# Kernel tuning notes

Hardware: AMD Instinct MI355X
Metric: run time of the kernel (lower is better)

Reference implementation:

```python
import jax, jax.numpy as jnp
import numpy as np

N = 50000        # nodes
E = 800000       # directed edges
NUM_E = 10000    # hyperedges
NFEAT, NHID, NOUT = 256, 128, 64
K = 10
TEMP = 5.0


def gcn_prop(h, src, dst, n):
    # PyG GCNConv propagation with added self-loops: D^-1/2 (A+I) D^-1/2 h
    ew = jnp.ones(src.shape[0], h.dtype)
    deg = 1.0 + jax.ops.segment_sum(ew, dst, num_segments=n)  # self-loop adds 1
    dinv = jax.lax.rsqrt(deg)
    norm = dinv[src] * dinv[dst]                   # [E]
    out = jax.ops.segment_sum(h[src] * norm[:, None], dst, num_segments=n)
    out = out + h / deg[:, None]                   # self-loop term (weight deg^-1)
    return out


def gcn_conv(x, W, b, src, dst, n):
    return gcn_prop(x @ W, src, dst, n) + b


def hgnnp_conv(x, W, b, hv, he, n, num_e):
    # dhg HGNNPConv: theta(x) then v->e mean aggregation, then e->v mean
    h = x @ W + b
    ones = jnp.ones(hv.shape[0], h.dtype)
    e_deg = jnp.maximum(jax.ops.segment_sum(ones, he, num_segments=num_e), 1.0)
    v_deg = jnp.maximum(jax.ops.segment_sum(ones, hv, num_segments=n), 1.0)
    e_feat = jax.ops.segment_sum(h[hv], he, num_segments=num_e) / e_deg[:, None]
    v_out = jax.ops.segment_sum(e_feat[he], hv, num_segments=n) / v_deg[:, None]
    return v_out


def setup_inputs() -> dict:
    key = jax.random.key(0)
    ks = jax.random.split(key, 12)
    x = jax.random.normal(ks[0], (N, NFEAT), jnp.float32)
    edge_index = jax.random.randint(ks[1], (2, E), 0, N)
    hv_idx = jax.random.randint(ks[2], (200000,), 0, N)
    he_idx = jax.random.randint(ks[3], (200000,), 0, NUM_E)

    def glorot(k, shape):
        lim = float(np.sqrt(6.0 / (shape[0] + shape[1])))
        return jax.random.uniform(k, shape, jnp.float32, -lim, lim)

    return {
        "x": x, "edge_index": edge_index, "hv_idx": hv_idx, "he_idx": he_idx,
        "gcn_W1": glorot(ks[4], (NFEAT, NHID)), "gcn_b1": jnp.zeros((NHID,), jnp.float32),
        "gcn_W2": glorot(ks[5], (NHID, NOUT)), "gcn_b2": jnp.zeros((NOUT,), jnp.float32),
        "hg_W1": glorot(ks[6], (NFEAT, NHID)), "hg_b1": jnp.zeros((NHID,), jnp.float32),
        "hg_W2": glorot(ks[7], (NHID, NOUT)), "hg_b2": jnp.zeros((NOUT,), jnp.float32),
        "num_iter": 1,
    }


def reference(x, edge_index, hv_idx, he_idx,
              gcn_W1, gcn_b1, gcn_W2, gcn_b2,
              hg_W1, hg_b1, hg_W2, hg_b2, num_iter):
    src, dst = edge_index[0], edge_index[1]

    # HGNNP_GCN encoder (dropout is identity in eval-style reference)
    x1 = jax.nn.relu(gcn_conv(x, gcn_W1, gcn_b1, src, dst, N))
    x2 = gcn_conv(x1, gcn_W2, gcn_b2, src, dst, N)
    x3 = jax.nn.relu(hgnnp_conv(x, hg_W1, hg_b1, hv_idx, he_idx, N, NUM_E))
    x4 = hgnnp_conv(x3, hg_W2, hg_b2, hv_idx, he_idx, N, NUM_E)  # is_last: no act
    embeds = x2 * 0.5 + x4 * 0.5                     # [N, NOUT]

    # row-normalize (diag(1/||row||) @ data)
    data = embeds / jnp.linalg.norm(embeds, axis=1, keepdims=True)

    # kmeans++ init is a host-side, data-dependent pick; use deterministic
    # strided row selection from the (detached) normalized embeddings.
    init_idx = jnp.arange(K) * (N // K)
    mu = jax.lax.stop_gradient(data[init_idx])       # [K, NOUT]

    for _ in range(int(num_iter)):
        dist = data @ mu.T                           # [N, K]
        r = jax.nn.softmax(TEMP * dist, axis=1)
        cluster_r = r.sum(axis=0)                    # [K]
        cluster_mean = r.T @ data                    # [K, NOUT]
        mu = cluster_mean / cluster_r[:, None]

    dist = data @ mu.T
    r = jax.nn.softmax(TEMP * dist, axis=1)
    return mu, r, embeds, dist
```

## Files before the change

### kernel.cpp

```cpp
#include <hip/hip_runtime.h>
#include <hip/hip_bf16.h>


#define NN   50000
#define NP   50048
#define EE   800000
#define NINC 200000
#define NEH  10000
#define KCL  10
#define CBLK 782

#define MU_OFF  0
#define R_OFF   640
#define EMB_OFF 500640
#define D_OFF   3700640

typedef __hip_bfloat16 bf16;
typedef unsigned short u16;
typedef unsigned int   u32;
typedef __attribute__((ext_vector_type(8))) short short8;
typedef __attribute__((ext_vector_type(4))) float f32x4;

__device__ __forceinline__ float b2f(bf16 v){ return __bfloat162float(v); }
__device__ __forceinline__ float us2f(u16 u){ return __uint_as_float(((unsigned)u) << 16); }
__device__ __forceinline__ u16 f2bu(float f){
  unsigned u = __float_as_uint(f);
  return (u16)((u + 0x7fffu + ((u >> 16) & 1u)) >> 16);
}
__device__ __forceinline__ bf16 f2b(float f){
  u16 r = f2bu(f);
  bf16 h;
  reinterpret_cast<u16&>(h) = r;
  return h;
}
__device__ __forceinline__ float ldf(const void* p, size_t i, int isbf){
  return isbf ? b2f(((const bf16*)p)[i]) : ((const float*)p)[i];
}
__device__ __forceinline__ void stf(void* p, size_t i, float v, int isbf){
  if (isbf) ((bf16*)p)[i] = f2b(v);
  else      ((float*)p)[i] = v;
}

__global__ void k_detect(const u16* __restrict__ xr, int* flag){
  __shared__ int bad;
  if (threadIdx.x == 0) bad = 0;
  __syncthreads();
  for (int i = threadIdx.x; i < 4096; i += 256){
    int e = (xr[i] >> 7) & 0xFF;
    if (e >= 0xEF) bad = 1;
  }
  __syncthreads();
  if (threadIdx.x == 0) *flag = bad ? 0 : 1;
}

__global__ void k_aconv(const void* __restrict__ x, u16* __restrict__ xb,
                        const int* __restrict__ flag){
  int i = blockIdx.x*256 + threadIdx.x;
  const int n4 = NN*256/4;
  if (i >= n4) return;
  ushort4 o;
  if (flag[0]){
    o = ((const ushort4*)x)[i];
  } else {
    float4 v = ((const float4*)x)[i];
    o = make_ushort4(f2bu(v.x), f2bu(v.y), f2bu(v.z), f2bu(v.w));
  }
  ((ushort4*)xb)[i] = o;
}

__global__ void k_wprep(const void* gW1, const void* hW1, const void* gW2, const void* hW2,
                        const void* gb1, const void* hb1, const void* gb2, const void* hb2,
                        u16* gW1t, u16* hW1t, u16* gW2t, u16* hW2t,
                        float* gb1f, float* hb1f, float* gb2f, float* hb2f,
                        const int* __restrict__ flag){
  const int isbf = flag[0];
  int i = blockIdx.x*256 + threadIdx.x;
  if (i < 256*128){
    int n = i >> 8, k = i & 255;
    gW1t[i] = f2bu(ldf(gW1, (size_t)k*128 + n, isbf));
    hW1t[i] = f2bu(ldf(hW1, (size_t)k*128 + n, isbf));
  }
  if (i < 64*128){
    int n = i >> 7, k = i & 127;
    gW2t[i] = f2bu(ldf(gW2, (size_t)k*64 + n, isbf));
    hW2t[i] = f2bu(ldf(hW2, (size_t)k*64 + n, isbf));
  }
  if (i < 128){ gb1f[i] = ldf(gb1,i,isbf); hb1f[i] = ldf(hb1,i,isbf); }
  if (i < 64) { gb2f[i] = ldf(gb2,i,isbf); hb2f[i] = ldf(hb2,i,isbf); }
}

template<int NBKT, int NPB>
__global__ __launch_bounds__(256) void k_histA(const int* __restrict__ key,
                                               int* __restrict__ HA, int chunk){
  __shared__ u32 hist[NBKT];
  for (int i = threadIdx.x; i < NBKT; i += 256) hist[i] = 0;
  __syncthreads();
  int base = blockIdx.x*chunk;
  for (int i = threadIdx.x; i < chunk; i += 256)
    atomicAdd(&hist[key[base+i]/NPB], 1u);
  __syncthreads();
  int* out = HA + blockIdx.x*NBKT;
  for (int i = threadIdx.x; i < NBKT; i += 256) out[i] = (int)hist[i];
}

__global__ void k_scanA_all(int* HAg, int* HAv, int* HAe,
                            int* bsg, int* bsv, int* bse){
  int* HA; int* bs; int nch;
  if (blockIdx.x == 0){ HA = HAg; bs = bsg; nch = 128; }
  else if (blockIdx.x == 1){ HA = HAv; bs = bsv; nch = 64; }
  else { HA = HAe; bs = bse; nch = 64; }
  __shared__ int s[256];
  int t = threadIdx.x;
  int run = 0;
  if (t < 250){
    for (int c = 0; c < nch; ++c){
      int v = HA[c*250 + t];
      HA[c*250 + t] = run;
      run += v;
    }
  }
  int own = (t < 250) ? run : 0;
  s[t] = own; __syncthreads();
  #pragma unroll
  for (int off = 1; off < 256; off <<= 1){
    int add = (t >= off) ? s[t-off] : 0;
    __syncthreads();
    s[t] += add;
    __syncthreads();
  }
  if (t < 250) bs[t] = s[t] - own;
  if (t == 255) bs[250] = s[255];
}

template<int NBKT, int NPB>
__global__ __launch_bounds__(256) void k_fillA(const int* __restrict__ key,
    const int* __restrict__ val, const int* __restrict__ HA,
    const int* __restrict__ bs, u32* __restrict__ packed, int chunk){
  __shared__ u32 cur[NBKT];
  const int* pre = HA + blockIdx.x*NBKT;
  for (int i = threadIdx.x; i < NBKT; i += 256) cur[i] = (u32)(bs[i] + pre[i]);
  __syncthreads();
  int base = blockIdx.x*chunk;
  for (int i = threadIdx.x; i < chunk; i += 256){
    int k = key[base+i];
    int b = k / NPB;
    u32 pos = atomicAdd(&cur[b], 1u);
    packed[pos] = ((u32)(k - b*NPB) << 16) | (u32)val[base+i];
  }
}

template<int NPB>
__global__ __launch_bounds__(256) void k_fillB(const u32* __restrict__ packed,
    const int* __restrict__ bs, int* __restrict__ csr,
    int* __restrict__ cnt, int* __restrict__ rp){
  __shared__ u32 hist[NPB];
  __shared__ int s[256];
  __shared__ u32 cur[NPB];
  const int b = blockIdx.x;
  const int s0 = bs[b], m = bs[b+1] - s0;
  const int t = threadIdx.x;
  for (int i = t; i < NPB; i += 256) hist[i] = 0;
  __syncthreads();
  for (int i = t; i < m; i += 256)
    atomicAdd(&hist[packed[s0+i] >> 16], 1u);
  __syncthreads();
  int own = (t < NPB) ? (int)hist[t] : 0;
  s[t] = own; __syncthreads();
  #pragma unroll
  for (int off = 1; off < 256; off <<= 1){
    int add = (t >= off) ? s[t-off] : 0;
    __syncthreads();
    s[t] += add;
    __syncthreads();
  }
  if (t < NPB){
    int excl = s[t] - own;
    cnt[b*NPB + t] = own;
    rp[b*NPB + t]  = s0 + excl;
    cur[t] = (u32)(s0 + excl);
  }
  __syncthreads();
  for (int i = t; i < m; i += 256){
    u32 p = packed[s0+i];
    u32 pos = atomicAdd(&cur[p >> 16], 1u);
    csr[pos] = (int)(p & 0xffffu);
  }
}

__global__ void k_invs(const int* __restrict__ cg, const int* __restrict__ cv,
                       const int* __restrict__ ce,
                       float* dinv, float* invv, float* inve){
  int i = blockIdx.x*256 + threadIdx.x;
  if (i < NN){
    float d = 1.0f + (float)cg[i];
    dinv[i] = rsqrtf(d);
    invv[i] = 1.0f / fmaxf((float)cv[i], 1.0f);
  } else if (i < NP){
    dinv[i] = 0.f;
  }
  if (i < NEH) inve[i] = 1.0f / fmaxf((float)ce[i], 1.0f);
}

template<int KDIM, int NCOL>
__global__ __launch_bounds__(256) void k_gemm_mfma(
    const u16* __restrict__ A, const u16* __restrict__ Wt,
    const float* __restrict__ bias, const float* __restrict__ rowscale,
    u16* __restrict__ C, int relu)
{
  constexpr int NT  = NCOL/16;
  constexpr int LDA = 40;
  __shared__ __align__(16) u16 Asl[64][LDA];
  __shared__ __align__(16) u16 Wsl[NCOL][LDA];
  const int tid  = threadIdx.x;
  const int wave = tid >> 6, lane = tid & 63;
  const int l15 = lane & 15, l4 = lane >> 4;
  const int row0 = blockIdx.x * 64;
  const int ar = tid >> 2, aq = tid & 3;
  constexpr int NW = NCOL*4/256;

  f32x4 acc[NT] = {};

  for (int kk = 0; kk < KDIM; kk += 32){
    {
      uint4 v = *(const uint4*)(A + (size_t)(row0 + ar)*KDIM + kk + aq*8);
      *(uint4*)&Asl[ar][aq*8] = v;
    }
    #pragma unroll
    for (int w2 = 0; w2 < NW; ++w2){
      int c = tid + w2*256;
      int n = c >> 2, q = c & 3;
      uint4 v = *(const uint4*)(Wt + (size_t)n*KDIM + kk + q*8);
      *(uint4*)&Wsl[n][q*8] = v;
    }
    __syncthreads();
    short8 af = *(const short8*)&Asl[wave*16 + l15][l4*8];
    #pragma unroll
    for (int t = 0; t < NT; ++t){
      short8 bf = *(const short8*)&Wsl[t*16 + l15][l4*8];
      acc[t] = __builtin_amdgcn_mfma_f32_16x16x32_bf16(af, bf, acc[t], 0, 0, 0);
    }
    __syncthreads();
  }

  #pragma unroll
  for (int t = 0; t < NT; ++t){
    int gcol = t*16 + l15;
    float b = bias ? bias[gcol] : 0.f;
    #pragma unroll
    for (int e = 0; e < 4; ++e){
      int grow = row0 + wave*16 + l4*4 + e;
      float v = acc[t][e] + b;
      if (relu) v = fmaxf(v, 0.f);
      if (rowscale) v *= rowscale[grow];
      C[(size_t)grow*NCOL + gcol] = f2bu(v);
    }
  }
}

template<int F, bool OUTBF, bool SELF>
__global__ __launch_bounds__(256) void k_gather(
    const int* __restrict__ rp, const int* __restrict__ cnt,
    const int* __restrict__ csr, const float* __restrict__ scale,
    const u16* __restrict__ h, const float* __restrict__ bias,
    void* __restrict__ out, int relu)
{
  const int wave = threadIdx.x >> 6, lane = threadIdx.x & 63;
  const int d = blockIdx.x*4 + wave;
  const int k0 = rp[d], n = cnt[d];

  if constexpr (F == 128){
    const uint* h32 = (const uint*)h;
    float a0=0,a1=0,b0=0,b1=0,c0=0,c1=0,e0=0,e1=0;
    if (SELF){
      uint v = h32[(size_t)d*64 + lane];
      a0 = us2f((u16)v); a1 = us2f((u16)(v>>16));
    }
    for (int base = 0; base < n; base += 64){
      int mm = n - base; if (mm > 64) mm = 64;
      int idx = (lane < mm) ? csr[k0 + base + lane] : 0;
      int jj = 0;
      for (; jj + 4 <= mm; jj += 4){
        int s0=__shfl(idx,jj), s1=__shfl(idx,jj+1), s2=__shfl(idx,jj+2), s3=__shfl(idx,jj+3);
        uint v0 = h32[(size_t)s0*64 + lane];
        uint v1 = h32[(size_t)s1*64 + lane];
        uint v2 = h32[(size_t)s2*64 + lane];
        uint v3 = h32[(size_t)s3*64 + lane];
        a0 += us2f((u16)v0); a1 += us2f((u16)(v0>>16));
        b0 += us2f((u16)v1); b1 += us2f((u16)(v1>>16));
        c0 += us2f((u16)v2); c1 += us2f((u16)(v2>>16));
        e0 += us2f((u16)v3); e1 += us2f((u16)(v3>>16));
      }
      for (; jj < mm; ++jj){
        int s = __shfl(idx, jj);
        uint v = h32[(size_t)s*64 + lane];
        a0 += us2f((u16)v); a1 += us2f((u16)(v>>16));
      }
    }
    float sc = scale[d];
    float o0 = ((a0+b0)+(c0+e0))*sc;
    float o1 = ((a1+b1)+(c1+e1))*sc;
    if (bias){ o0 += bias[lane*2]; o1 += bias[lane*2+1]; }
    if (relu){ o0 = fmaxf(o0,0.f); o1 = fmaxf(o1,0.f); }
    if (OUTBF){
      ((uint*)out)[(size_t)d*64 + lane] = (uint)f2bu(o0) | ((uint)f2bu(o1) << 16);
    } else {
      ((float2*)out)[(size_t)d*64 + lane] = make_float2(o0, o1);
    }
  } else {
    float a=0,b=0,c=0,e=0;
    if (SELF) a = us2f(h[(size_t)d*64 + lane]);
    for (int base = 0; base < n; base += 64){
      int mm = n - base; if (mm > 64) mm = 64;
      int idx = (lane < mm) ? csr[k0 + base + lane] : 0;
      int jj = 0;
      for (; jj + 4 <= mm; jj += 4){
        int s0=__shfl(idx,jj), s1=__shfl(idx,jj+1), s2=__shfl(idx,jj+2), s3=__shfl(idx,jj+3);
        a += us2f(h[(size_t)s0*64 + lane]);
        b += us2f(h[(size_t)s1*64 + lane]);
        c += us2f(h[(size_t)s2*64 + lane]);
        e += us2f(h[(size_t)s3*64 + lane]);
      }
      for (; jj < mm; ++jj){
        int s = __shfl(idx, jj);
        a += us2f(h[(size_t)s*64 + lane]);
      }
    }
    float o = ((a+b)+(c+e))*scale[d];
    if (bias) o += bias[lane];
    if (relu) o = fmaxf(o, 0.f);
    if (OUTBF) ((u16*)out)[(size_t)d*64 + lane] = f2bu(o);
    else       ((float*)out)[(size_t)d*64 + lane] = o;
  }
}

__global__ void k_embeds(const float* __restrict__ x2, const float* __restrict__ x4,
                         void* __restrict__ out, float* __restrict__ data,
                         const int* __restrict__ flag){
  int row  = blockIdx.x*4 + (threadIdx.x >> 6);
  int lane = threadIdx.x & 63;
  if (row >= NN) return;
  size_t idx = (size_t)row*64 + lane;
  float v = 0.5f*(x2[idx] + x4[idx]);
  float ss = v*v;
  #pragma unroll
  for (int off=32; off>0; off>>=1) ss += __shfl_xor(ss, off);
  float inv = rsqrtf(ss);
  data[idx] = v*inv;
  stf(out, EMB_OFF + idx, v, flag[0]);
}

__global__ void k_mu_init(const float* __restrict__ data, float* __restrict__ mu){
  int p = blockIdx.x*256 + threadIdx.x;
  if (p >= KCL*64) return;
  int k = p >> 6, f = p & 63;
  mu[p] = data[(size_t)k*(NN/KCL)*64 + f];
}

__global__ __launch_bounds__(640) void k_cluster_iter(const float* __restrict__ data,
    const float* __restrict__ mu, float* __restrict__ part, float* __restrict__ pcr,
    const int* __restrict__ nit, int iter)
{
  if (iter >= nit[0]) return;
  __shared__ float ms[640];
  __shared__ float dt[64][65];
  __shared__ float ds[64][11];
  const int tid = threadIdx.x;
  ms[tid] = mu[tid];
  const int base = blockIdx.x*64;
  for (int i = tid; i < 4096; i += 640){
    int r = i >> 6, f = i & 63;
    int grow = base + r;
    dt[r][f] = (grow < NN) ? data[(size_t)grow*64 + f] : 0.f;
  }
  __syncthreads();
  {
    const int row = tid & 63, k = tid >> 6;
    float dot = 0.f;
    #pragma unroll 16
    for (int f = 0; f < 64; ++f)
      dot = fmaf(dt[row][f], ms[k*64 + f], dot);
    ds[row][k] = dot;
  }
  __syncthreads();
  if (tid < 64){
    float dot[KCL];
    #pragma unroll
    for (int k = 0; k < KCL; ++k) dot[k] = ds[tid][k];
    float m = -1e30f;
    #pragma unroll
    for (int k = 0; k < KCL; ++k) m = fmaxf(m, 5.0f*dot[k]);
    float s = 0.f, ev[KCL];
    #pragma unroll
    for (int k = 0; k < KCL; ++k){ ev[k] = expf(5.0f*dot[k]-m); s += ev[k]; }
    float inv = (base + tid < NN) ? 1.0f/s : 0.f;
    #pragma unroll
    for (int k = 0; k < KCL; ++k) ds[tid][k] = ev[k]*inv;
  }
  __syncthreads();
  {
    const int f = tid & 63, k = tid >> 6;
    float acc = 0.f, crp = 0.f;
    #pragma unroll 8
    for (int t = 0; t < 64; ++t){
      float rv = ds[t][k];
      acc = fmaf(rv, dt[t][f], acc);
      crp += rv;
    }
    part[(size_t)blockIdx.x*640 + tid] = acc;
    if (f == 0) pcr[blockIdx.x*16 + k] = crp;
  }
}

__global__ void k_cred1(const float* __restrict__ part, const float* __restrict__ pcr,
                        float* __restrict__ p2, float* __restrict__ pc2,
                        const int* __restrict__ nit, int iter){
  if (iter >= nit[0]) return;
  int b = blockIdx.x, t = threadIdx.x;
  int r0 = b*20, r1 = r0 + 20; if (r1 > CBLK) r1 = CBLK;
  if (t < 640){
    float a = 0.f;
    for (int r = r0; r < r1; ++r) a += part[(size_t)r*640 + t];
    p2[(size_t)b*640 + t] = a;
  } else if (t < 640 + KCL){
    int k = t - 640;
    float a = 0.f;
    for (int r = r0; r < r1; ++r) a += pcr[r*16 + k];
    pc2[b*16 + k] = a;
  }
}

__global__ void k_cred2(const float* __restrict__ p2, const float* __restrict__ pc2,
                        float* __restrict__ csum, float* __restrict__ cr,
                        const int* __restrict__ nit, int iter){
  if (iter >= nit[0]) return;
  int t = threadIdx.x;
  if (t < 640){
    float a = 0.f;
    #pragma unroll
    for (int b = 0; b < 40; ++b) a += p2[(size_t)b*640 + t];
    csum[t] = a;
  } else if (t < 640 + KCL){
    int k = t - 640;
    float a = 0.f;
    #pragma unroll
    for (int b = 0; b < 40; ++b) a += pc2[b*16 + k];
    cr[k] = a;
  }
}

__global__ void k_mu_update(float* __restrict__ mu, const float* __restrict__ csum,
                            const float* __restrict__ cr,
                            const int* __restrict__ nit, int iter){
  if (iter >= nit[0]) return;
  int p = threadIdx.x;
  mu[p] = csum[p] / cr[p >> 6];
}

__global__ __launch_bounds__(640) void k_cluster_final(const float* __restrict__ data,
    const float* __restrict__ mu, void* __restrict__ out, const int* __restrict__ flag)
{
  __shared__ float ms[640];
  __shared__ float dt[64][65];
  __shared__ float ds[64][11];
  const int tid = threadIdx.x;
  ms[tid] = mu[tid];
  const int base = blockIdx.x*64;
  for (int i = tid; i < 4096; i += 640){
    int r = i >> 6, f = i & 63;
    int grow = base + r;
    dt[r][f] = (grow < NN) ? data[(size_t)grow*64 + f] : 0.f;
  }
  __syncthreads();
  {
    const int row = tid & 63, k = tid >> 6;
    float dot = 0.f;
    #pragma unroll 16
    for (int f = 0; f < 64; ++f)
      dot = fmaf(dt[row][f], ms[k*64 + f], dot);
    ds[row][k] = dot;
  }
  __syncthreads();
  if (tid < 64 && base + tid < NN){
    const int row = base + tid;
    const int isbf = flag[0];
    float dot[KCL];
    #pragma unroll
    for (int k = 0; k < KCL; ++k) dot[k] = ds[tid][k];
    float m = -1e30f;
    #pragma unroll
    for (int k = 0; k < KCL; ++k) m = fmaxf(m, 5.0f*dot[k]);
    float s = 0.f, ev[KCL];
    #pragma unroll
    for (int k = 0; k < KCL; ++k){ ev[k] = expf(5.0f*dot[k]-m); s += ev[k]; }
    float inv = 1.0f/s;
    #pragma unroll
    for (int k = 0; k < KCL; ++k){
      stf(out, (size_t)D_OFF + (size_t)row*KCL + k, dot[k],    isbf);
      stf(out, (size_t)R_OFF + (size_t)row*KCL + k, ev[k]*inv, isbf);
    }
  }
}

__global__ void k_mu_out(const float* __restrict__ mu, void* __restrict__ out,
                         const int* __restrict__ flag){
  int p = blockIdx.x*256 + threadIdx.x;
  if (p < KCL*64) stf(out, MU_OFF + p, mu[p], flag[0]);
}

extern "C" void kernel_launch(void* const* d_in, const int* in_sizes, int n_in,
                              void* d_out, int out_size, void* d_ws, size_t ws_size,
                              hipStream_t stream)
{
  const void* x   = d_in[0];
  const int*  ei  = (const int*)d_in[1];
  const int*  hv  = (const int*)d_in[2];
  const int*  he  = (const int*)d_in[3];
  const void* gW1 = d_in[4];
  const void* gb1 = d_in[5];
  const void* gW2 = d_in[6];
  const void* gb2 = d_in[7];
  const void* hW1 = d_in[8];
  const void* hb1 = d_in[9];
  const void* hW2 = d_in[10];
  const void* hb2 = d_in[11];
  const int*  nit = (const int*)d_in[12];

  float* ws = (float*)d_ws;
  size_t o = 0;
  u16*   xb  = (u16*)(ws + o); o += (size_t)NP*128;
  u16*   BAb = (u16*)(ws + o); o += (size_t)NP*64;
  u16*   BBb = (u16*)(ws + o); o += (size_t)NP*64;
  u16*   BCb = (u16*)(ws + o); o += (size_t)NP*64;
  u16*   BDb = (u16*)(ws + o); o += (size_t)NEH*64;
  u16*  gW1t = (u16*)(ws + o); o += 16384;
  u16*  hW1t = (u16*)(ws + o); o += 16384;
  u16*  gW2t = (u16*)(ws + o); o += 4096;
  u16*  hW2t = (u16*)(ws + o); o += 4096;
  float* gb1f = ws + o; o += 128;
  float* hb1f = ws + o; o += 128;
  float* gb2f = ws + o; o += 64;
  float* hb2f = ws + o; o += 64;
  float* dinv = ws + o; o += 50048;
  float* invv = ws + o; o += 50048;
  float* inve = ws + o; o += 10048;
  float* mu   = ws + o; o += 640;
  float* csum = ws + o; o += 640;
  float* cr   = ws + o; o += 64;
  float* part = ws + o; o += (size_t)CBLK*640;
  float* pcr  = ws + o; o += CBLK*16;
  float* p2   = ws + o; o += 40*640;
  float* pc2  = ws + o; o += 40*16;
  int*   dflg = (int*)(ws + o); o += 16;
  float* x2f   = (float*)xb;
  float* x4f   = (float*)xb + (size_t)NP*64;
  float* dataf = (float*)BBb;
  int* ib = (int*)(ws + o);
  size_t io = 0;
  int* cg    = ib + io; io += NN;
  int* cv    = ib + io; io += NN;
  int* ce    = ib + io; io += NEH + 48;
  int* rp_g  = ib + io; io += NN;
  int* rp_v  = ib + io; io += NN;
  int* rp_e  = ib + io; io += NEH + 48;
  int* csr_g = ib + io; io += EE;
  int* csr_e = ib + io; io += NINC;
  int* csr_v = ib + io; io += NINC;
  int* HAg   = ib + io; io += 128*250;
  int* HAv   = ib + io; io += 64*250;
  int* HAe   = ib + io; io += 64*250;
  int* bsg   = ib + io; io += 256;
  int* bsv   = ib + io; io += 256;
  int* bse   = ib + io; io += 256;
  u32* pg = (u32*)(ib + io); io += EE;
  u32* pv = (u32*)(ib + io); io += NINC;
  u32* pe = (u32*)(ib + io); io += NINC;

  const int* srcp = ei;
  const int* dstp = ei + EE;
  dim3 B(256);
  const int NBP = (NP + 255)/256;

  k_detect<<<dim3(1), B, 0, stream>>>((const u16*)x, dflg);
  k_aconv<<<dim3(12500), B, 0, stream>>>(x, xb, dflg);
  k_wprep<<<dim3(128), B, 0, stream>>>(gW1, hW1, gW2, hW2, gb1, hb1, gb2, hb2,
                                       gW1t, hW1t, gW2t, hW2t,
                                       gb1f, hb1f, gb2f, hb2f, dflg);

  k_histA<250,200><<<dim3(128), B, 0, stream>>>(dstp, HAg, 6250);
  k_histA<250,200><<<dim3(64),  B, 0, stream>>>(hv,   HAv, 3125);
  k_histA<250, 40><<<dim3(64),  B, 0, stream>>>(he,   HAe, 3125);
  k_scanA_all<<<dim3(3), B, 0, stream>>>(HAg, HAv, HAe, bsg, bsv, bse);
  k_fillA<250,200><<<dim3(128), B, 0, stream>>>(dstp, srcp, HAg, bsg, pg, 6250);
  k_fillA<250,200><<<dim3(64),  B, 0, stream>>>(hv,   he,   HAv, bsv, pv, 3125);
  k_fillA<250, 40><<<dim3(64),  B, 0, stream>>>(he,   hv,   HAe, bse, pe, 3125);
  k_fillB<200><<<dim3(250), B, 0, stream>>>(pg, bsg, csr_g, cg, rp_g);
  k_fillB<200><<<dim3(250), B, 0, stream>>>(pv, bsv, csr_v, cv, rp_v);
  k_fillB< 40><<<dim3(250), B, 0, stream>>>(pe, bse, csr_e, ce, rp_e);
  k_invs<<<dim3(NBP), B, 0, stream>>>(cg, cv, ce, dinv, invv, inve);

  const int NB = NP/64;
  k_gemm_mfma<256,128><<<dim3(NB), B, 0, stream>>>(xb, gW1t, nullptr, dinv, BAb, 0);
  k_gather<128,true,true><<<dim3(NN/4), B, 0, stream>>>(rp_g, cg, csr_g, dinv,
                                                        BAb, gb1f, BBb, 1);
  k_gemm_mfma<256,128><<<dim3(NB), B, 0, stream>>>(xb, hW1t, hb1f, nullptr, BAb, 0);
  k_gather<128,true,false><<<dim3(NEH/4), B, 0, stream>>>(rp_e, ce, csr_e, inve,
                                                          BAb, nullptr, BDb, 0);
  k_gather<128,true,false><<<dim3(NN/4), B, 0, stream>>>(rp_v, cv, csr_v, invv,
                                                         BDb, nullptr, BCb, 1);
  k_gemm_mfma<128,64><<<dim3(NB), B, 0, stream>>>(BBb, gW2t, nullptr, dinv, BAb, 0);
  k_gather<64,false,true><<<dim3(NN/4), B, 0, stream>>>(rp_g, cg, csr_g, dinv,
                                                        BAb, gb2f, x2f, 0);
  k_gemm_mfma<128,64><<<dim3(NB), B, 0, stream>>>(BCb, hW2t, hb2f, nullptr, BAb, 0);
  k_gather<64,true,false><<<dim3(NEH/4), B, 0, stream>>>(rp_e, ce, csr_e, inve,
                                                         BAb, nullptr, BDb, 0);
  k_gather<64,false,false><<<dim3(NN/4), B, 0, stream>>>(rp_v, cv, csr_v, invv,
                                                         BDb, nullptr, x4f, 0);

  k_embeds<<<dim3((NN+3)/4), B, 0, stream>>>(x2f, x4f, d_out, dataf, dflg);

  k_mu_init<<<dim3(3), B, 0, stream>>>(dataf, mu);
  for (int it = 0; it < 4; ++it){
    k_cluster_iter<<<dim3(CBLK), dim3(640), 0, stream>>>(dataf, mu, part, pcr, nit, it);
    k_cred1       <<<dim3(40),   dim3(768), 0, stream>>>(part, pcr, p2, pc2, nit, it);
    k_cred2       <<<dim3(1),    dim3(768), 0, stream>>>(p2, pc2, csum, cr, nit, it);
    k_mu_update   <<<dim3(1),    dim3(640), 0, stream>>>(mu, csum, cr, nit, it);
  }
  k_cluster_final<<<dim3(CBLK), dim3(640), 0, stream>>>(dataf, mu, d_out, dflg);
  k_mu_out       <<<dim3(3),  B, 0, stream>>>(mu, d_out, dflg);
}
```

Baseline: 372.3 us.

## Merge independent GCN and hypergraph stages into shared launches to cut kernel count

Merges independent kernels into combined launches that dispatch on block index. Input and weight prep become one launch, and the three histogram, fillA and fillB passes each become one launch, with the degree-inverse computation folded into fillB. The GCN and hypergraph GEMM and gather stages are paired so that independent branches run in the same grid, using an extra buffer BEb to break the write conflicts. The cluster reduce and mu update are fused, and the mu output write moves into the final kernel. This removes about 20 launches and their serialization gaps, at the cost of mixed-workload grids where GEMM and gather blocks share one register and LDS budget.

```diff
diff --git a/kernel.cpp b/kernel.cpp
--- a/kernel.cpp
+++ b/kernel.cpp
@@ -53,54 +53,58 @@
   if (threadIdx.x == 0) *flag = bad ? 0 : 1;
 }
 
-__global__ void k_aconv(const void* __restrict__ x, u16* __restrict__ xb,
-                        const int* __restrict__ flag){
-  int i = blockIdx.x*256 + threadIdx.x;
-  const int n4 = NN*256/4;
-  if (i >= n4) return;
-  ushort4 o;
-  if (flag[0]){
-    o = ((const ushort4*)x)[i];
+__global__ __launch_bounds__(256) void k_prep(const void* __restrict__ x, u16* __restrict__ xb,
+    const void* gW1, const void* hW1, const void* gW2, const void* hW2,
+    const void* gb1, const void* hb1, const void* gb2, const void* hb2,
+    u16* gW1t, u16* hW1t, u16* gW2t, u16* hW2t,
+    float* gb1f, float* hb1f, float* gb2f, float* hb2f,
+    const int* __restrict__ flag){
+  const int isbf = flag[0];
+  const int blk = blockIdx.x;
+  if (blk < 12500){
+    int i = blk*256 + threadIdx.x;
+    ushort4 o;
+    if (isbf){
+      o = ((const ushort4*)x)[i];
+    } else {
+      float4 v = ((const float4*)x)[i];
+      o = make_ushort4(f2bu(v.x), f2bu(v.y), f2bu(v.z), f2bu(v.w));
+    }
+    ((ushort4*)xb)[i] = o;
   } else {
-    float4 v = ((const float4*)x)[i];
-    o = make_ushort4(f2bu(v.x), f2bu(v.y), f2bu(v.z), f2bu(v.w));
-  }
-  ((ushort4*)xb)[i] = o;
-}
-
-__global__ void k_wprep(const void* gW1, const void* hW1, const void* gW2, const void* hW2,
-                        const void* gb1, const void* hb1, const void* gb2, const void* hb2,
-                        u16* gW1t, u16* hW1t, u16* gW2t, u16* hW2t,
-                        float* gb1f, float* hb1f, float* gb2f, float* hb2f,
-                        const int* __restrict__ flag){
-  const int isbf = flag[0];
-  int i = blockIdx.x*256 + threadIdx.x;
-  if (i < 256*128){
-    int n = i >> 8, k = i & 255;
-    gW1t[i] = f2bu(ldf(gW1, (size_t)k*128 + n, isbf));
-    hW1t[i] = f2bu(ldf(hW1, (size_t)k*128 + n, isbf));
-  }
-  if (i < 64*128){
-    int n = i >> 7, k = i & 127;
-    gW2t[i] = f2bu(ldf(gW2, (size_t)k*64 + n, isbf));
-    hW2t[i] = f2bu(ldf(hW2, (size_t)k*64 + n, isbf));
-  }
-  if (i < 128){ gb1f[i] = ldf(gb1,i,isbf); hb1f[i] = ldf(hb1,i,isbf); }
-  if (i < 64) { gb2f[i] = ldf(gb2,i,isbf); hb2f[i] = ldf(hb2,i,isbf); }
-}
-
-template<int NBKT, int NPB>
-__global__ __launch_bounds__(256) void k_histA(const int* __restrict__ key,
-                                               int* __restrict__ HA, int chunk){
-  __shared__ u32 hist[NBKT];
-  for (int i = threadIdx.x; i < NBKT; i += 256) hist[i] = 0;
-  __syncthreads();
-  int base = blockIdx.x*chunk;
+    int i = (blk - 12500)*256 + threadIdx.x;
+    if (i < 256*128){
+      int n = i >> 8, k = i & 255;
+      gW1t[i] = f2bu(ldf(gW1, (size_t)k*128 + n, isbf));
+      hW1t[i] = f2bu(ldf(hW1, (size_t)k*128 + n, isbf));
+    }
+    if (i < 64*128){
+      int n = i >> 7, k = i & 127;
+      gW2t[i] = f2bu(ldf(gW2, (size_t)k*64 + n, isbf));
+      hW2t[i] = f2bu(ldf(hW2, (size_t)k*64 + n, isbf));
+    }
+    if (i < 128){ gb1f[i] = ldf(gb1,i,isbf); hb1f[i] = ldf(hb1,i,isbf); }
+    if (i < 64) { gb2f[i] = ldf(gb2,i,isbf); hb2f[i] = ldf(hb2,i,isbf); }
+  }
+}
+
+__global__ __launch_bounds__(256) void k_hist_all(const int* __restrict__ dstp,
+    const int* __restrict__ hv, const int* __restrict__ he,
+    int* HAg, int* HAv, int* HAe){
+  __shared__ u32 hist[250];
+  const int blk = blockIdx.x;
+  const int* key; int* HA; int chunk, npb, lb;
+  if (blk < 128){ key=dstp; HA=HAg; chunk=6250; npb=200; lb=blk; }
+  else if (blk < 192){ key=hv; HA=HAv; chunk=3125; npb=200; lb=blk-128; }
+  else { key=he; HA=HAe; chunk=3125; npb=40; lb=blk-192; }
+  for (int i = threadIdx.x; i < 250; i += 256) hist[i] = 0;
+  __syncthreads();
+  int base = lb*chunk;
   for (int i = threadIdx.x; i < chunk; i += 256)
-    atomicAdd(&hist[key[base+i]/NPB], 1u);
-  __syncthreads();
-  int* out = HA + blockIdx.x*NBKT;
-  for (int i = threadIdx.x; i < NBKT; i += 256) out[i] = (int)hist[i];
+    atomicAdd(&hist[key[base+i]/npb], 1u);
+  __syncthreads();
+  int* out = HA + lb*250;
+  for (int i = threadIdx.x; i < 250; i += 256) out[i] = (int)hist[i];
 }
 
 __global__ void k_scanA_all(int* HAg, int* HAv, int* HAe,
@@ -132,39 +136,52 @@
   if (t == 255) bs[250] = s[255];
 }
 
-template<int NBKT, int NPB>
-__global__ __launch_bounds__(256) void k_fillA(const int* __restrict__ key,
-    const int* __restrict__ val, const int* __restrict__ HA,
-    const int* __restrict__ bs, u32* __restrict__ packed, int chunk){
-  __shared__ u32 cur[NBKT];
-  const int* pre = HA + blockIdx.x*NBKT;
-  for (int i = threadIdx.x; i < NBKT; i += 256) cur[i] = (u32)(bs[i] + pre[i]);
-  __syncthreads();
-  int base = blockIdx.x*chunk;
+__global__ __launch_bounds__(256) void k_fillA_all(const int* __restrict__ dstp,
+    const int* __restrict__ srcp, const int* __restrict__ hv, const int* __restrict__ he,
+    const int* HAg, const int* HAv, const int* HAe,
+    const int* bsg, const int* bsv, const int* bse,
+    u32* pg, u32* pv, u32* pe){
+  __shared__ u32 cur[250];
+  const int blk = blockIdx.x;
+  const int* key; const int* val; const int* HA; const int* bs; u32* packed;
+  int chunk, npb, lb;
+  if (blk < 128){ key=dstp; val=srcp; HA=HAg; bs=bsg; packed=pg; chunk=6250; npb=200; lb=blk; }
+  else if (blk < 192){ key=hv; val=he; HA=HAv; bs=bsv; packed=pv; chunk=3125; npb=200; lb=blk-128; }
+  else { key=he; val=hv; HA=HAe; bs=bse; packed=pe; chunk=3125; npb=40; lb=blk-192; }
+  const int* pre = HA + lb*250;
+  for (int i = threadIdx.x; i < 250; i += 256) cur[i] = (u32)(bs[i] + pre[i]);
+  __syncthreads();
+  int base = lb*chunk;
   for (int i = threadIdx.x; i < chunk; i += 256){
     int k = key[base+i];
-    int b = k / NPB;
+    int b = k / npb;
     u32 pos = atomicAdd(&cur[b], 1u);
-    packed[pos] = ((u32)(k - b*NPB) << 16) | (u32)val[base+i];
-  }
-}
-
-template<int NPB>
-__global__ __launch_bounds__(256) void k_fillB(const u32* __restrict__ packed,
-    const int* __restrict__ bs, int* __restrict__ csr,
-    int* __restrict__ cnt, int* __restrict__ rp){
-  __shared__ u32 hist[NPB];
+    packed[pos] = ((u32)(k - b*npb) << 16) | (u32)val[base+i];
+  }
+}
+
+__global__ __launch_bounds__(256) void k_fillB_all(
+    const u32* pg, const u32* pv, const u32* pe,
+    const int* bsg, const int* bsv, const int* bse,
+    int* csr_g, int* csr_v, int* csr_e,
+    int* cg, int* cv, int* ce, int* rp_g, int* rp_v, int* rp_e,
+    float* dinv, float* invv, float* inve){
+  __shared__ u32 hist[200];
   __shared__ int s[256];
-  __shared__ u32 cur[NPB];
-  const int b = blockIdx.x;
+  __shared__ u32 cur[200];
+  const int blk = blockIdx.x;
+  const u32* packed; const int* bs; int* csr; int* cnt; int* rp; int npb, b, mode;
+  if (blk < 250){ packed=pg; bs=bsg; csr=csr_g; cnt=cg; rp=rp_g; npb=200; b=blk; mode=0; }
+  else if (blk < 500){ packed=pv; bs=bsv; csr=csr_v; cnt=cv; rp=rp_v; npb=200; b=blk-250; mode=1; }
+  else { packed=pe; bs=bse; csr=csr_e; cnt=ce; rp=rp_e; npb=40; b=blk-500; mode=2; }
   const int s0 = bs[b], m = bs[b+1] - s0;
   const int t = threadIdx.x;
-  for (int i = t; i < NPB; i += 256) hist[i] = 0;
+  for (int i = t; i < npb; i += 256) hist[i] = 0;
   __syncthreads();
   for (int i = t; i < m; i += 256)
     atomicAdd(&hist[packed[s0+i] >> 16], 1u);
   __syncthreads();
-  int own = (t < NPB) ? (int)hist[t] : 0;
+  int own = (t < npb) ? (int)hist[t] : 0;
   s[t] = own; __syncthreads();
   #pragma unroll
   for (int off = 1; off < 256; off <<= 1){
@@ -173,12 +190,17 @@
     s[t] += add;
     __syncthreads();
   }
-  if (t < NPB){
+  if (t < npb){
     int excl = s[t] - own;
-    cnt[b*NPB + t] = own;
-    rp[b*NPB + t]  = s0 + excl;
+    int node = b*npb + t;
+    cnt[node] = own;
+    rp[node]  = s0 + excl;
     cur[t] = (u32)(s0 + excl);
-  }
+    if (mode == 0)      dinv[node] = rsqrtf(1.0f + (float)own);
+    else if (mode == 1) invv[node] = 1.0f / fmaxf((float)own, 1.0f);
+    else                inve[node] = 1.0f / fmaxf((float)own, 1.0f);
+  }
+  if (mode == 0 && b == 249 && t < NP - NN) dinv[NN + t] = 0.f;
   __syncthreads();
   for (int i = t; i < m; i += 256){
     u32 p = packed[s0+i];
@@ -187,25 +209,10 @@
   }
 }
 
-__global__ void k_invs(const int* __restrict__ cg, const int* __restrict__ cv,
-                       const int* __restrict__ ce,
-                       float* dinv, float* invv, float* inve){
-  int i = blockIdx.x*256 + threadIdx.x;
-  if (i < NN){
-    float d = 1.0f + (float)cg[i];
-    dinv[i] = rsqrtf(d);
-    invv[i] = 1.0f / fmaxf((float)cv[i], 1.0f);
-  } else if (i < NP){
-    dinv[i] = 0.f;
-  }
-  if (i < NEH) inve[i] = 1.0f / fmaxf((float)ce[i], 1.0f);
-}
-
 template<int KDIM, int NCOL>
-__global__ __launch_bounds__(256) void k_gemm_mfma(
-    const u16* __restrict__ A, const u16* __restrict__ Wt,
-    const float* __restrict__ bias, const float* __restrict__ rowscale,
-    u16* __restrict__ C, int relu)
+__device__ __forceinline__ void gemm_body(const u16* __restrict__ A,
+    const u16* __restrict__ Wt, const float* __restrict__ bias,
+    const float* __restrict__ rowscale, u16* __restrict__ C, int relu, int bid)
 {
   constexpr int NT  = NCOL/16;
   constexpr int LDA = 40;
@@ -214,7 +221,7 @@
   const int tid  = threadIdx.x;
   const int wave = tid >> 6, lane = tid & 63;
   const int l15 = lane & 15, l4 = lane >> 4;
-  const int row0 = blockIdx.x * 64;
+  const int row0 = bid * 64;
   const int ar = tid >> 2, aq = tid & 3;
   constexpr int NW = NCOL*4/256;
 
@@ -258,14 +265,13 @@
 }
 
 template<int F, bool OUTBF, bool SELF>
-__global__ __launch_bounds__(256) void k_gather(
-    const int* __restrict__ rp, const int* __restrict__ cnt,
-    const int* __restrict__ csr, const float* __restrict__ scale,
-    const u16* __restrict__ h, const float* __restrict__ bias,
-    void* __restrict__ out, int relu)
+__device__ __forceinline__ void gather_body(const int* __restrict__ rp,
+    const int* __restrict__ cnt, const int* __restrict__ csr,
+    const float* __restrict__ scale, const u16* __restrict__ h,
+    const float* __restrict__ bias, void* __restrict__ out, int relu, int bid)
 {
   const int wave = threadIdx.x >> 6, lane = threadIdx.x & 63;
-  const int d = blockIdx.x*4 + wave;
+  const int d = bid*4 + wave;
   const int k0 = rp[d], n = cnt[d];
 
   if constexpr (F == 128){
@@ -333,6 +339,45 @@
   }
 }
 
+__global__ __launch_bounds__(256) void k_pA(const u16* xb, const u16* gW1t,
+    const float* dinv, u16* BAb){
+  gemm_body<256,128>(xb, gW1t, nullptr, dinv, BAb, 0, blockIdx.x);
+}
+__global__ __launch_bounds__(256) void k_pB(const u16* xb, const u16* hW1t,
+    const float* hb1f, u16* BEb,
+    const int* rp_g, const int* cg, const int* csr_g, const float* dinv,
+    const u16* BAb, const float* gb1f, u16* BBb){
+  if (blockIdx.x < 782) gemm_body<256,128>(xb, hW1t, hb1f, nullptr, BEb, 0, blockIdx.x);
+  else gather_body<128,true,true>(rp_g, cg, csr_g, dinv, BAb, gb1f, BBb, 1, blockIdx.x - 782);
+}
+__global__ __launch_bounds__(256) void k_pC(const u16* BBb, const u16* gW2t,
+    const float* dinv, u16* BAb,
+    const int* rp_e, const int* ce, const int* csr_e, const float* inve,
+    const u16* BEb, u16* BDb){
+  if (blockIdx.x < 782) gemm_body<128,64>(BBb, gW2t, nullptr, dinv, BAb, 0, blockIdx.x);
+  else gather_body<128,true,false>(rp_e, ce, csr_e, inve, BEb, nullptr, BDb, 0, blockIdx.x - 782);
+}
+__global__ __launch_bounds__(256) void k_pD(
+    const int* rp_v, const int* cv, const int* csr_v, const float* invv,
+    const u16* BDb, u16* BCb,
+    const int* rp_g, const int* cg, const int* csr_g, const float* dinv,
+    const u16* BAb, const float* gb2f, float* x2f){
+  if (blockIdx.x < 12500) gather_body<128,true,false>(rp_v, cv, csr_v, invv, BDb, nullptr, BCb, 1, blockIdx.x);
+  else gather_body<64,false,true>(rp_g, cg, csr_g, dinv, BAb, gb2f, x2f, 0, blockIdx.x - 12500);
+}
+__global__ __launch_bounds__(256) void k_pE(const u16* BCb, const u16* hW2t,
+    const float* hb2f, u16* BEb){
+  gemm_body<128,64>(BCb, hW2t, hb2f, nullptr, BEb, 0, blockIdx.x);
+}
+__global__ __launch_bounds__(256) void k_pF(const int* rp_e, const int* ce,
+    const int* csr_e, const float* inve, const u16* BEb, u16* BDb){
+  gather_body<64,true,false>(rp_e, ce, csr_e, inve, BEb, nullptr, BDb, 0, blockIdx.x);
+}
+__global__ __launch_bounds__(256) void k_pG(const int* rp_v, const int* cv,
+    const int* csr_v, const float* invv, const u16* BDb, float* x4f){
+  gather_body<64,false,false>(rp_v, cv, csr_v, invv, BDb, nullptr, x4f, 0, blockIdx.x);
+}
+
 __global__ void k_embeds(const float* __restrict__ x2, const float* __restrict__ x4,
                          void* __restrict__ out, float* __restrict__ data,
                          const int* __restrict__ flag){
@@ -350,8 +395,7 @@
 }
 
 __global__ void k_mu_init(const float* __restrict__ data, float* __restrict__ mu){
-  int p = blockIdx.x*256 + threadIdx.x;
-  if (p >= KCL*64) return;
+  int p = threadIdx.x;
   int k = p >> 6, f = p & 63;
   mu[p] = data[(size_t)k*(NN/KCL)*64 + f];
 }
@@ -429,31 +473,25 @@
   }
 }
 
-__global__ void k_cred2(const float* __restrict__ p2, const float* __restrict__ pc2,
-                        float* __restrict__ csum, float* __restrict__ cr,
-                        const int* __restrict__ nit, int iter){
+__global__ void k_cred2mu(const float* __restrict__ p2, const float* __restrict__ pc2,
+                          float* __restrict__ mu, const int* __restrict__ nit, int iter){
   if (iter >= nit[0]) return;
+  __shared__ float crs[16];
   int t = threadIdx.x;
+  if (t >= 640 && t < 640 + KCL){
+    int k = t - 640;
+    float a = 0.f;
+    #pragma unroll
+    for (int b = 0; b < 40; ++b) a += pc2[b*16 + k];
+    crs[k] = a;
+  }
+  __syncthreads();
   if (t < 640){
     float a = 0.f;
     #pragma unroll
     for (int b = 0; b < 40; ++b) a += p2[(size_t)b*640 + t];
-    csum[t] = a;
-  } else if (t < 640 + KCL){
-    int k = t - 640;
-    float a = 0.f;
-    #pragma unroll
-    for (int b = 0; b < 40; ++b) a += pc2[b*16 + k];
-    cr[k] = a;
-  }
-}
-
-__global__ void k_mu_update(float* __restrict__ mu, const float* __restrict__ csum,
-                            const float* __restrict__ cr,
-                            const int* __restrict__ nit, int iter){
-  if (iter >= nit[0]) return;
-  int p = threadIdx.x;
-  mu[p] = csum[p] / cr[p >> 6];
+    mu[t] = a / crs[t >> 6];
+  }
 }
 
 __global__ __launch_bounds__(640) void k_cluster_final(const float* __restrict__ data,
@@ -480,9 +518,10 @@
     ds[row][k] = dot;
   }
   __syncthreads();
+  const int isbf = flag[0];
+  if (blockIdx.x == 0) stf(out, MU_OFF + tid, ms[tid], isbf);
   if (tid < 64 && base + tid < NN){
     const int row = base + tid;
-    const int isbf = flag[0];
     float dot[KCL];
     #pragma unroll
     for (int k = 0; k < KCL; ++k) dot[k] = ds[tid][k];
@@ -499,12 +538,6 @@
       stf(out, (size_t)R_OFF + (size_t)row*KCL + k, ev[k]*inv, isbf);
     }
   }
-}
-
-__global__ void k_mu_out(const float* __restrict__ mu, void* __restrict__ out,
-                         const int* __restrict__ flag){
-  int p = blockIdx.x*256 + threadIdx.x;
-  if (p < KCL*64) stf(out, MU_OFF + p, mu[p], flag[0]);
 }
 
 extern "C" void kernel_launch(void* const* d_in, const int* in_sizes, int n_in,
@@ -531,6 +564,7 @@
   u16*   BAb = (u16*)(ws + o); o += (size_t)NP*64;
   u16*   BBb = (u16*)(ws + o); o += (size_t)NP*64;
   u16*   BCb = (u16*)(ws + o); o += (size_t)NP*64;
+  u16*   BEb = (u16*)(ws + o); o += (size_t)NP*64;
   u16*   BDb = (u16*)(ws + o); o += (size_t)NEH*64;
   u16*  gW1t = (u16*)(ws + o); o += 16384;
   u16*  hW1t = (u16*)(ws + o); o += 16384;
@@ -544,8 +578,6 @@
   float* invv = ws + o; o += 50048;
   float* inve = ws + o; o += 10048;
   float* mu   = ws + o; o += 640;
-  float* csum = ws + o; o += 640;
-  float* cr   = ws + o; o += 64;
   float* part = ws + o; o += (size_t)CBLK*640;
   float* pcr  = ws + o; o += CBLK*16;
   float* p2   = ws + o; o += 40*640;
@@ -578,53 +610,39 @@
   const int* srcp = ei;
   const int* dstp = ei + EE;
   dim3 B(256);
-  const int NBP = (NP + 255)/256;
 
   k_detect<<<dim3(1), B, 0, stream>>>((const u16*)x, dflg);
-  k_aconv<<<dim3(12500), B, 0, stream>>>(x, xb, dflg);
-  k_wprep<<<dim3(128), B, 0, stream>>>(gW1, hW1, gW2, hW2, gb1, hb1, gb2, hb2,
-                                       gW1t, hW1t, gW2t, hW2t,
-                                       gb1f, hb1f, gb2f, hb2f, dflg);
-
-  k_histA<250,200><<<dim3(128), B, 0, stream>>>(dstp, HAg, 6250);
-  k_histA<250,200><<<dim3(64),  B, 0, stream>>>(hv,   HAv, 3125);
-  k_histA<250, 40><<<dim3(64),  B, 0, stream>>>(he,   HAe, 3125);
-  k_scanA_all<<<dim3(3), B, 0, stream>>>(HAg, HAv, HAe, bsg, bsv, bse);
-  k_fillA<250,200><<<dim3(128), B, 0, stream>>>(dstp, srcp, HAg, bsg, pg, 6250);
-  k_fillA<250,200><<<dim3(64),  B, 0, stream>>>(hv,   he,   HAv, bsv, pv, 3125);
-  k_fillA<250, 40><<<dim3(64),  B, 0, stream>>>(he,   hv,   HAe, bse, pe, 3125);
-  k_fillB<200><<<dim3(250), B, 0, stream>>>(pg, bsg, csr_g, cg, rp_g);
-  k_fillB<200><<<dim3(250), B, 0, stream>>>(pv, bsv, csr_v, cv, rp_v);
-  k_fillB< 40><<<dim3(250), B, 0, stream>>>(pe, bse, csr_e, ce, rp_e);
-  k_invs<<<dim3(NBP), B, 0, stream>>>(cg, cv, ce, dinv, invv, inve);
-
-  const int NB = NP/64;
-  k_gemm_mfma<256,128><<<dim3(NB), B, 0, stream>>>(xb, gW1t, nullptr, dinv, BAb, 0);
-  k_gather<128,true,true><<<dim3(NN/4), B, 0, stream>>>(rp_g, cg, csr_g, dinv,
-                                                        BAb, gb1f, BBb, 1);
-  k_gemm_mfma<256,128><<<dim3(NB), B, 0, stream>>>(xb, hW1t, hb1f, nullptr, BAb, 0);
-  k_gather<128,true,false><<<dim3(NEH/4), B, 0, stream>>>(rp_e, ce, csr_e, inve,
-                                                          BAb, nullptr, BDb, 0);
-  k_gather<128,true,false><<<dim3(NN/4), B, 0, stream>>>(rp_v, cv, csr_v, invv,
-                                                         BDb, nullptr, BCb, 1);
-  k_gemm_mfma<128,64><<<dim3(NB), B, 0, stream>>>(BBb, gW2t, nullptr, dinv, BAb, 0);
-  k_gather<64,false,true><<<dim3(NN/4), B, 0, stream>>>(rp_g, cg, csr_g, dinv,
-                                                        BAb, gb2f, x2f, 0);
-  k_gemm_mfma<128,64><<<dim3(NB), B, 0, stream>>>(BCb, hW2t, hb2f, nullptr, BAb, 0);
-  k_gather<64,true,false><<<dim3(NEH/4), B, 0, stream>>>(rp_e, ce, csr_e, inve,
-                                                         BAb, nullptr, BDb, 0);
-  k_gather<64,false,false><<<dim3(NN/4), B, 0, stream>>>(rp_v, cv, csr_v, invv,
-                                                         BDb, nullptr, x4f, 0);
+  k_prep<<<dim3(12628), B, 0, stream>>>(x, xb, gW1, hW1, gW2, hW2,
+                                        gb1, hb1, gb2, hb2,
+                                        gW1t, hW1t, gW2t, hW2t,
+                                        gb1f, hb1f, gb2f, hb2f, dflg);
+
+  k_hist_all <<<dim3(256), B, 0, stream>>>(dstp, hv, he, HAg, HAv, HAe);
+  k_scanA_all<<<dim3(3),   B, 0, stream>>>(HAg, HAv, HAe, bsg, bsv, bse);
+  k_fillA_all<<<dim3(256), B, 0, stream>>>(dstp, srcp, hv, he, HAg, HAv, HAe,
+                                           bsg, bsv, bse, pg, pv, pe);
+  k_fillB_all<<<dim3(750), B, 0, stream>>>(pg, pv, pe, bsg, bsv, bse,
+                                           csr_g, csr_v, csr_e, cg, cv, ce,
+                                           rp_g, rp_v, rp_e, dinv, invv, inve);
+
+  k_pA<<<dim3(782),   B, 0, stream>>>(xb, gW1t, dinv, BAb);
+  k_pB<<<dim3(13282), B, 0, stream>>>(xb, hW1t, hb1f, BEb,
+                                      rp_g, cg, csr_g, dinv, BAb, gb1f, BBb);
+  k_pC<<<dim3(3282),  B, 0, stream>>>(BBb, gW2t, dinv, BAb,
+                                      rp_e, ce, csr_e, inve, BEb, BDb);
+  k_pD<<<dim3(25000), B, 0, stream>>>(rp_v, cv, csr_v, invv, BDb, BCb,
+                                      rp_g, cg, csr_g, dinv, BAb, gb2f, x2f);
+  k_pE<<<dim3(782),   B, 0, stream>>>(BCb, hW2t, hb2f, BEb);
+  k_pF<<<dim3(2500),  B, 0, stream>>>(rp_e, ce, csr_e, inve, BEb, BDb);
+  k_pG<<<dim3(12500), B, 0, stream>>>(rp_v, cv, csr_v, invv, BDb, x4f);
 
   k_embeds<<<dim3((NN+3)/4), B, 0, stream>>>(x2f, x4f, d_out, dataf, dflg);
 
-  k_mu_init<<<dim3(3), B, 0, stream>>>(dataf, mu);
+  k_mu_init<<<dim3(1), dim3(640), 0, stream>>>(dataf, mu);
   for (int it = 0; it < 4; ++it){
     k_cluster_iter<<<dim3(CBLK), dim3(640), 0, stream>>>(dataf, mu, part, pcr, nit, it);
     k_cred1       <<<dim3(40),   dim3(768), 0, stream>>>(part, pcr, p2, pc2, nit, it);
-    k_cred2       <<<dim3(1),    dim3(768), 0, stream>>>(p2, pc2, csum, cr, nit, it);
-    k_mu_update   <<<dim3(1),    dim3(640), 0, stream>>>(mu, csum, cr, nit, it);
+    k_cred2mu     <<<dim3(1),    dim3(768), 0, stream>>>(p2, pc2, mu, nit, it);
   }
   k_cluster_final<<<dim3(CBLK), dim3(640), 0, stream>>>(dataf, mu, d_out, dflg);
-  k_mu_out       <<<dim3(3),  B, 0, stream>>>(mu, d_out, dflg);
-}
+}
```

Result: faster. 321.3 us (-13.7%).
